# Performance work log

Hardware: AMD Instinct MI355X
Metric: run time of the kernel (lower is better)

Reference implementation:

```python
import jax, jax.numpy as jnp
import numpy as np

NUM_HEADS = 4
EPS = 1e-5  # GroupNorm default eps


def setup_inputs() -> dict:
    key = jax.random.key(0)
    ks = jax.random.split(key, 4)
    B, T, C, H, W = 4, 8, 128, 96, 96
    x = jax.random.normal(ks[0], (B, T, C, H, W), jnp.float32)
    pos_enc = jax.random.normal(ks[1], (1, 16, C, 1, 1), jnp.float32) * 0.02
    norm_w = jnp.ones((C,), jnp.float32)
    norm_b = jnp.zeros((C,), jnp.float32)
    qkv_w = jax.random.normal(ks[2], (3 * C, C), jnp.float32) * (1.0 / np.sqrt(C))
    proj_w = jax.random.normal(ks[3], (C, C), jnp.float32) * (1.0 / np.sqrt(C))
    return {"x": x, "pos_enc": pos_enc, "norm_w": norm_w, "norm_b": norm_b,
            "qkv_w": qkv_w, "proj_w": proj_w}


def reference(x, pos_enc, norm_w, norm_b, qkv_w, proj_w):
    B, T, C, H, W = x.shape
    nh = NUM_HEADS
    hd = C // nh
    scale = hd ** -0.5

    x = x + pos_enc[:, :T]

    # GroupNorm(1, C): normalize over (C,H,W) per (B,T) sample, biased var
    mean = x.mean(axis=(2, 3, 4), keepdims=True)
    var = x.var(axis=(2, 3, 4), keepdims=True)
    xn = (x - mean) * jax.lax.rsqrt(var + EPS)
    xn = xn * norm_w[None, None, :, None, None] + norm_b[None, None, :, None, None]

    # 1x1 conv -> matmul over channel dim; d = 3C
    qkv = jnp.einsum('btchw,dc->btdhw', xn, qkv_w)
    qkv = qkv.reshape(B, T, 3, nh, hd, H, W)
    q, k, v = qkv[:, :, 0], qkv[:, :, 1], qkv[:, :, 2]  # [B,T,nh,hd,H,W]

    # per-pixel temporal attention: scores [B,nh,H,W,T,T]
    attn = jnp.einsum('btndhw,bsndhw->bnhwts', q, k) * scale
    attn = jax.nn.softmax(attn, axis=-1)

    # only the last query row is kept (out[..., -1, :] in the original)
    out = jnp.einsum('bnhws,bsndhw->bndhw', attn[..., -1, :], v)
    out = out.reshape(B, C, H, W)
    return jnp.einsum('bchw,dc->bdhw', out, proj_w)
```

## Files before the change

kernel.cpp:

```cpp
#include <hip/hip_runtime.h>
#include <math.h>

#define BB 4
#define TT 8
#define CC 128
#define HWW 9216
#define NPG 1179648.0f
#define EPS 1e-5f
#define SCALE 0.17677669529663687f
#define SCALE2 0.2550181765195206f

#define WS_PART 0
#define WS_A    8192
#define WS_B    12288

typedef __attribute__((ext_vector_type(4))) float f32x4;

__global__ __launch_bounds__(256) void stats_kernel(
    const float* __restrict__ x, const float* __restrict__ pe,
    float* __restrict__ part)
{
    const int bid = blockIdx.x;
    const int g = bid >> 7, c = bid & 127;
    const int t = g & 7;
    const int tid = threadIdx.x;
    const float pec = pe[t * CC + c];
    const float4* row = (const float4*)(x + ((size_t)g * CC + c) * HWW);
    float s1 = 0.f, s2 = 0.f;
    #pragma unroll
    for (int i = 0; i < 9; ++i) {
        float4 v = row[tid + i * 256];
        float a = v.x + pec, b = v.y + pec, cc2 = v.z + pec, d = v.w + pec;
        s1 += (a + b) + (cc2 + d);
        s2 += (a * a + b * b) + (cc2 * cc2 + d * d);
    }
    for (int off = 32; off; off >>= 1) {
        s1 += __shfl_down(s1, off);
        s2 += __shfl_down(s2, off);
    }
    __shared__ float red[8];
    const int wid = tid >> 6, lane = tid & 63;
    if (lane == 0) { red[wid] = s1; red[4 + wid] = s2; }
    __syncthreads();
    if (tid == 0) {
        part[bid * 2 + 0] = red[0] + red[1] + red[2] + red[3];
        part[bid * 2 + 1] = red[4] + red[5] + red[6] + red[7];
    }
}

__global__ __launch_bounds__(128) void finalize_kernel(
    const float* __restrict__ pe, const float* __restrict__ nw,
    const float* __restrict__ nb, float* ws)
{
    const int g = blockIdx.x;
    const int c = threadIdx.x;
    const float* part = ws + WS_PART + g * 256;
    float s1 = part[c * 2 + 0];
    float s2 = part[c * 2 + 1];
    for (int off = 32; off; off >>= 1) {
        s1 += __shfl_down(s1, off);
        s2 += __shfl_down(s2, off);
    }
    __shared__ float r[4];
    const int wid = c >> 6, lane = c & 63;
    if (lane == 0) { r[wid] = s1; r[2 + wid] = s2; }
    __syncthreads();
    const float inv = 1.0f / NPG;
    const float mean = (r[0] + r[1]) * inv;
    const float var  = (r[2] + r[3]) * inv - mean * mean;
    const float rstd = rsqrtf(var + EPS);
    const int t = g & 7;
    const float a = rstd * nw[c];
    ws[WS_A + g * CC + c] = a;
    ws[WS_B + g * CC + c] = (pe[t * CC + c] - mean) * a + nb[c];
}

__global__ __launch_bounds__(1024, 4) void fused7_kernel(
    const float* __restrict__ x, const float* __restrict__ ws,
    const float* __restrict__ qkv_w, const float* __restrict__ proj_w,
    float* __restrict__ out)
{
    __shared__ __align__(16) float bufA[CC * 64];
    __shared__ __align__(16) float bufB[CC * 64];

    const int tid  = threadIdx.x;
    const int lane = tid & 63;
    const int w    = tid >> 6;
    const int wu   = __builtin_amdgcn_readfirstlane(w);
    const int n    = wu >> 2;
    const int hq   = wu & 3;
    const int b    = blockIdx.y;
    const int hw0  = blockIdx.x * 64;

    const int r  = tid >> 3;
    const int k8 = (tid & 7) * 8;

    float ar[8], br[8];
    #pragma unroll
    for (int t = 0; t < 8; ++t) {
        ar[t] = ws[WS_A + (b * TT + t) * CC + r];
        br[t] = ws[WS_B + (b * TT + t) * CC + r];
    }

    const float* xrow = x + ((size_t)(b * TT) * CC + r) * HWW + hw0 + k8;

    f32x4 rg0, rg1;
    auto ldtile = [&](int t) {
        const float* p = xrow + (size_t)t * CC * HWW;
        rg0 = *(const f32x4*)(p);
        rg1 = *(const f32x4*)(p + 4);
    };
    auto wrtile = [&](float a, float bb2, float* dst) {
        f32x4 f0, f1;
        f0.x = fmaf(rg0.x, a, bb2); f0.y = fmaf(rg0.y, a, bb2);
        f0.z = fmaf(rg0.z, a, bb2); f0.w = fmaf(rg0.w, a, bb2);
        f1.x = fmaf(rg1.x, a, bb2); f1.y = fmaf(rg1.y, a, bb2);
        f1.z = fmaf(rg1.z, a, bb2); f1.w = fmaf(rg1.w, a, bb2);
        *(f32x4*)&dst[r * 64 + k8]     = f0;
        *(f32x4*)&dst[r * 64 + k8 + 4] = f1;
    };

    float u[32];
    auto score = [&](const float* buf) {
        float s0 = 0.f, s1 = 0.f, s2 = 0.f, s3 = 0.f;
        #pragma unroll
        for (int j = 0; j < 32; j += 4) {
            s0 = fmaf(u[j + 0], buf[(hq * 32 + j + 0) * 64 + lane], s0);
            s1 = fmaf(u[j + 1], buf[(hq * 32 + j + 1) * 64 + lane], s1);
            s2 = fmaf(u[j + 2], buf[(hq * 32 + j + 2) * 64 + lane], s2);
            s3 = fmaf(u[j + 3], buf[(hq * 32 + j + 3) * 64 + lane], s3);
        }
        return (s0 + s1) + (s2 + s3);
    };

    ldtile(7);
    wrtile(ar[7], br[7], bufA);
    __syncthreads();

    {
        const float* Wq = qkv_w + (n * 32 + hq * 8) * CC;
        float q7[8] = {0.f,0.f,0.f,0.f,0.f,0.f,0.f,0.f};
        for (int c0 = 0; c0 < CC; c0 += 8) {
            float xv[8];
            #pragma unroll
            for (int i = 0; i < 8; ++i)
                xv[i] = bufA[(c0 + i) * 64 + lane];
            #pragma unroll
            for (int d = 0; d < 8; ++d) {
                #pragma unroll
                for (int i = 0; i < 8; ++i)
                    q7[d] = fmaf(Wq[d * CC + c0 + i], xv[i], q7[d]);
            }
        }
        #pragma unroll
        for (int d = 0; d < 8; ++d)
            bufB[(n * 32 + hq * 8 + d) * 64 + lane] = q7[d];
    }
    __syncthreads();

    ldtile(0);

    #pragma unroll
    for (int j = 0; j < 32; ++j) u[j] = 0.f;
    {
        const float* Wk = qkv_w + (CC + n * 32) * CC + hq * 32;
        for (int d = 0; d < 32; ++d) {
            const float qv = bufB[(n * 32 + d) * 64 + lane];
            #pragma unroll
            for (int j = 0; j < 32; ++j)
                u[j] = fmaf(Wk[d * CC + j], qv, u[j]);
        }
    }
    __syncthreads();

    float ps[8];
    wrtile(ar[0], br[0], bufB);
    ps[7] = score(bufA);
    ldtile(1);
    __syncthreads();

    #pragma unroll
    for (int t = 0; t < 7; ++t) {
        const float* curb = (t & 1) ? bufA : bufB;
        float* othb = (t & 1) ? bufB : bufA;
        if (t < 6) {
            if (t == 0) wrtile(ar[1], br[1], othb);
            if (t == 1) wrtile(ar[2], br[2], othb);
            if (t == 2) wrtile(ar[3], br[3], othb);
            if (t == 3) wrtile(ar[4], br[4], othb);
            if (t == 4) wrtile(ar[5], br[5], othb);
            if (t == 5) wrtile(ar[6], br[6], othb);
        }
        if (t < 5) ldtile(t + 2);
        ps[t] = score(curb);
        __syncthreads();
    }

    ldtile(0);
    #pragma unroll
    for (int t = 0; t < 8; ++t)
        bufA[(wu * 8 + t) * 64 + lane] = ps[t];
    __syncthreads();

    float wt[8];
    {
        float sreg[8];
        #pragma unroll
        for (int t = 0; t < 8; ++t)
            sreg[t] = (bufA[((n * 4 + 0) * 8 + t) * 64 + lane] +
                       bufA[((n * 4 + 1) * 8 + t) * 64 + lane]) +
                      (bufA[((n * 4 + 2) * 8 + t) * 64 + lane] +
                       bufA[((n * 4 + 3) * 8 + t) * 64 + lane]);
        float m = fmaxf(fmaxf(fmaxf(sreg[0], sreg[1]), fmaxf(sreg[2], sreg[3])),
                        fmaxf(fmaxf(sreg[4], sreg[5]), fmaxf(sreg[6], sreg[7])));
        float l = 0.f;
        #pragma unroll
        for (int t = 0; t < 8; ++t) { wt[t] = exp2f((sreg[t] - m) * SCALE2); l += wt[t]; }
        const float invl = 1.0f / l;
        #pragma unroll
        for (int t = 0; t < 8; ++t) wt[t] *= invl;
    }
    __syncthreads();

    float xb[32];
    #pragma unroll
    for (int j = 0; j < 32; ++j) xb[j] = 0.f;
    #pragma unroll
    for (int t = 0; t < 8; ++t) {
        float* wb = (t & 1) ? bufB : bufA;
        {
            if (t == 0) wrtile(ar[0], br[0], wb);
            if (t == 1) wrtile(ar[1], br[1], wb);
            if (t == 2) wrtile(ar[2], br[2], wb);
            if (t == 3) wrtile(ar[3], br[3], wb);
            if (t == 4) wrtile(ar[4], br[4], wb);
            if (t == 5) wrtile(ar[5], br[5], wb);
            if (t == 6) wrtile(ar[6], br[6], wb);
            if (t == 7) wrtile(ar[7], br[7], wb);
        }
        if (t < 7) ldtile(t + 1);
        if (t >= 1) {
            const float* rb = (t & 1) ? bufA : bufB;
            const float wc = wt[t - 1];
            #pragma unroll
            for (int j = 0; j < 32; ++j)
                xb[j] = fmaf(rb[(hq * 32 + j) * 64 + lane], wc, xb[j]);
        }
        __syncthreads();
    }
    {
        const float wc = wt[7];
        #pragma unroll
        for (int j = 0; j < 32; ++j)
            xb[j] = fmaf(bufB[(hq * 32 + j) * 64 + lane], wc, xb[j]);
    }
    __syncthreads();

    {
        const float* Wv = qkv_w + (2 * CC + n * 32) * CC + hq * 32;
        float vprev[8];
        #pragma unroll
        for (int gi = 0; gi < 4; ++gi) {
            float vp[8];
            #pragma unroll
            for (int d = 0; d < 8; ++d) {
                float s0 = 0.f, s1 = 0.f, s2 = 0.f, s3 = 0.f;
                const float* Wr = Wv + (gi * 8 + d) * CC;
                #pragma unroll
                for (int c = 0; c < 32; c += 4) {
                    s0 = fmaf(Wr[c + 0], xb[c + 0], s0);
                    s1 = fmaf(Wr[c + 1], xb[c + 1], s1);
                    s2 = fmaf(Wr[c + 2], xb[c + 2], s2);
                    s3 = fmaf(Wr[c + 3], xb[c + 3], s3);
                }
                vp[d] = (s0 + s1) + (s2 + s3);
            }
            if (hq == 1) {
                #pragma unroll
                for (int d = 0; d < 8; ++d)
                    bufB[(n * 32 + gi * 8 + d) * 64 + lane] = vp[d];
            }
            if (hq == 3) {
                #pragma unroll
                for (int d = 0; d < 8; ++d)
                    bufA[(n * 32 + gi * 8 + d) * 64 + lane] = vp[d];
            }
            if (gi > 0) {
                if (hq == 0) {
                    #pragma unroll
                    for (int d = 0; d < 8; ++d)
                        bufB[(n * 32 + (gi - 1) * 8 + d) * 64 + lane] += vprev[d];
                }
                if (hq == 2) {
                    #pragma unroll
                    for (int d = 0; d < 8; ++d)
                        bufA[(n * 32 + (gi - 1) * 8 + d) * 64 + lane] += vprev[d];
                }
            }
            #pragma unroll
            for (int d = 0; d < 8; ++d) vprev[d] = vp[d];
            __syncthreads();
        }
        if (hq == 0) {
            #pragma unroll
            for (int d = 0; d < 8; ++d)
                bufB[(n * 32 + 24 + d) * 64 + lane] += vprev[d];
        }
        if (hq == 2) {
            #pragma unroll
            for (int d = 0; d < 8; ++d)
                bufA[(n * 32 + 24 + d) * 64 + lane] += vprev[d];
        }
    }
    __syncthreads();

    float y[8];
    #pragma unroll
    for (int e = 0; e < 8; ++e) y[e] = 0.f;
    for (int c0 = 0; c0 < CC; c0 += 16) {
        float vv[16];
        #pragma unroll
        for (int i = 0; i < 16; ++i)
            vv[i] = bufB[(c0 + i) * 64 + lane] + bufA[(c0 + i) * 64 + lane];
        #pragma unroll
        for (int e = 0; e < 8; ++e) {
            const float* Pr = proj_w + (wu * 8 + e) * CC + c0;
            #pragma unroll
            for (int i = 0; i < 16; ++i)
                y[e] = fmaf(Pr[i], vv[i], y[e]);
        }
    }
    const size_t ob = (size_t)(b * CC + wu * 8) * HWW + hw0 + lane;
    #pragma unroll
    for (int e = 0; e < 8; ++e)
        out[ob + (size_t)e * HWW] = y[e];
}

extern "C" void kernel_launch(void* const* d_in, const int* in_sizes, int n_in,
                              void* d_out, int out_size, void* d_ws, size_t ws_size,
                              hipStream_t stream) {
    const float* x      = (const float*)d_in[0];
    const float* pe     = (const float*)d_in[1];
    const float* nw     = (const float*)d_in[2];
    const float* nb     = (const float*)d_in[3];
    const float* qkv_w  = (const float*)d_in[4];
    const float* proj_w = (const float*)d_in[5];
    float* out = (float*)d_out;
    float* ws  = (float*)d_ws;

    stats_kernel<<<4096, 256, 0, stream>>>(x, pe, ws + WS_PART);
    finalize_kernel<<<32, 128, 0, stream>>>(pe, nw, nb, ws);
    fused7_kernel<<<dim3(HWW / 64, BB), 1024, 0, stream>>>(x, ws, qkv_w, proj_w, out);
}
```

Before: 413.9 us.

## Transpose LDS tiles to pixel-major with XOR swizzle and vectorized reads

Shared-memory tiles change from channel-major to pixel-major rows of 128 channels, with an XOR swizzle on 4-float groups. Every consumer (score, q/k projections, weighted sum, v partial sums, output projection) now reads 128-bit vectors instead of scalar LDS loads. The per-timestep normalization coefficients are loaded alongside each x tile instead of kept in 16 registers. The launch-bounds occupancy hint goes from 4 to 8, which presses register allocation. The tile writes become eight scattered scalar stores, which may add bank conflicts on the write side.

```diff
diff --git a/kernel.cpp b/kernel.cpp
--- a/kernel.cpp
+++ b/kernel.cpp
@@ -75,13 +75,13 @@
     ws[WS_B + g * CC + c] = (pe[t * CC + c] - mean) * a + nb[c];
 }
 
-__global__ __launch_bounds__(1024, 4) void fused7_kernel(
+__global__ __launch_bounds__(1024, 8) void fused8_kernel(
     const float* __restrict__ x, const float* __restrict__ ws,
     const float* __restrict__ qkv_w, const float* __restrict__ proj_w,
     float* __restrict__ out)
 {
-    __shared__ __align__(16) float bufA[CC * 64];
-    __shared__ __align__(16) float bufB[CC * 64];
+    __shared__ __align__(16) float bufA[64 * CC];
+    __shared__ __align__(16) float bufB[64 * CC];
 
     const int tid  = threadIdx.x;
     const int lane = tid & 63;
@@ -92,69 +92,76 @@
     const int b    = blockIdx.y;
     const int hw0  = blockIdx.x * 64;
 
+    const int pg   = (lane >> 3) & 7;
+    const int rowb = lane * 128;
+
     const int r  = tid >> 3;
     const int k8 = (tid & 7) * 8;
 
-    float ar[8], br[8];
-    #pragma unroll
-    for (int t = 0; t < 8; ++t) {
-        ar[t] = ws[WS_A + (b * TT + t) * CC + r];
-        br[t] = ws[WS_B + (b * TT + t) * CC + r];
-    }
-
     const float* xrow = x + ((size_t)(b * TT) * CC + r) * HWW + hw0 + k8;
+    const float* Arow = ws + WS_A + (b * TT) * CC + r;
+    const float* Brow = ws + WS_B + (b * TT) * CC + r;
 
     f32x4 rg0, rg1;
+    float sa, sb;
     auto ldtile = [&](int t) {
         const float* p = xrow + (size_t)t * CC * HWW;
         rg0 = *(const f32x4*)(p);
         rg1 = *(const f32x4*)(p + 4);
+        sa = Arow[t * CC];
+        sb = Brow[t * CC];
     };
-    auto wrtile = [&](float a, float bb2, float* dst) {
-        f32x4 f0, f1;
-        f0.x = fmaf(rg0.x, a, bb2); f0.y = fmaf(rg0.y, a, bb2);
-        f0.z = fmaf(rg0.z, a, bb2); f0.w = fmaf(rg0.w, a, bb2);
-        f1.x = fmaf(rg1.x, a, bb2); f1.y = fmaf(rg1.y, a, bb2);
-        f1.z = fmaf(rg1.z, a, bb2); f1.w = fmaf(rg1.w, a, bb2);
-        *(f32x4*)&dst[r * 64 + k8]     = f0;
-        *(f32x4*)&dst[r * 64 + k8 + 4] = f1;
+    auto wrtile = [&](float* dst) {
+        const int base = k8 * 128 + ((((r >> 2) ^ ((k8 >> 3) & 7)) << 2) | (r & 3));
+        dst[base + 0 * 128] = fmaf(rg0.x, sa, sb);
+        dst[base + 1 * 128] = fmaf(rg0.y, sa, sb);
+        dst[base + 2 * 128] = fmaf(rg0.z, sa, sb);
+        dst[base + 3 * 128] = fmaf(rg0.w, sa, sb);
+        dst[base + 4 * 128] = fmaf(rg1.x, sa, sb);
+        dst[base + 5 * 128] = fmaf(rg1.y, sa, sb);
+        dst[base + 6 * 128] = fmaf(rg1.z, sa, sb);
+        dst[base + 7 * 128] = fmaf(rg1.w, sa, sb);
     };
 
     float u[32];
     auto score = [&](const float* buf) {
         float s0 = 0.f, s1 = 0.f, s2 = 0.f, s3 = 0.f;
         #pragma unroll
-        for (int j = 0; j < 32; j += 4) {
-            s0 = fmaf(u[j + 0], buf[(hq * 32 + j + 0) * 64 + lane], s0);
-            s1 = fmaf(u[j + 1], buf[(hq * 32 + j + 1) * 64 + lane], s1);
-            s2 = fmaf(u[j + 2], buf[(hq * 32 + j + 2) * 64 + lane], s2);
-            s3 = fmaf(u[j + 3], buf[(hq * 32 + j + 3) * 64 + lane], s3);
+        for (int jj = 0; jj < 8; ++jj) {
+            f32x4 v = *(const f32x4*)&buf[rowb + (((hq * 8 + jj) ^ pg) << 2)];
+            s0 = fmaf(u[jj * 4 + 0], v.x, s0);
+            s1 = fmaf(u[jj * 4 + 1], v.y, s1);
+            s2 = fmaf(u[jj * 4 + 2], v.z, s2);
+            s3 = fmaf(u[jj * 4 + 3], v.w, s3);
         }
         return (s0 + s1) + (s2 + s3);
     };
 
     ldtile(7);
-    wrtile(ar[7], br[7], bufA);
+    wrtile(bufA);
     __syncthreads();
 
     {
         const float* Wq = qkv_w + (n * 32 + hq * 8) * CC;
         float q7[8] = {0.f,0.f,0.f,0.f,0.f,0.f,0.f,0.f};
-        for (int c0 = 0; c0 < CC; c0 += 8) {
-            float xv[8];
-            #pragma unroll
-            for (int i = 0; i < 8; ++i)
-                xv[i] = bufA[(c0 + i) * 64 + lane];
+        #pragma unroll
+        for (int cc = 0; cc < 32; ++cc) {
+            f32x4 xv = *(const f32x4*)&bufA[rowb + ((cc ^ pg) << 2)];
             #pragma unroll
             for (int d = 0; d < 8; ++d) {
-                #pragma unroll
-                for (int i = 0; i < 8; ++i)
-                    q7[d] = fmaf(Wq[d * CC + c0 + i], xv[i], q7[d]);
-            }
-        }
-        #pragma unroll
-        for (int d = 0; d < 8; ++d)
-            bufB[(n * 32 + hq * 8 + d) * 64 + lane] = q7[d];
+                const float* Wr = Wq + d * CC + cc * 4;
+                q7[d] = fmaf(Wr[0], xv.x, q7[d]);
+                q7[d] = fmaf(Wr[1], xv.y, q7[d]);
+                q7[d] = fmaf(Wr[2], xv.z, q7[d]);
+                q7[d] = fmaf(Wr[3], xv.w, q7[d]);
+            }
+        }
+        const int c0 = n * 8 + hq * 2;
+        f32x4 e0, e1;
+        e0.x = q7[0]; e0.y = q7[1]; e0.z = q7[2]; e0.w = q7[3];
+        e1.x = q7[4]; e1.y = q7[5]; e1.z = q7[6]; e1.w = q7[7];
+        *(f32x4*)&bufB[rowb + ((c0 ^ pg) << 2)]       = e0;
+        *(f32x4*)&bufB[rowb + (((c0 + 1) ^ pg) << 2)] = e1;
     }
     __syncthreads();
 
@@ -164,17 +171,26 @@
     for (int j = 0; j < 32; ++j) u[j] = 0.f;
     {
         const float* Wk = qkv_w + (CC + n * 32) * CC + hq * 32;
-        for (int d = 0; d < 32; ++d) {
-            const float qv = bufB[(n * 32 + d) * 64 + lane];
-            #pragma unroll
-            for (int j = 0; j < 32; ++j)
-                u[j] = fmaf(Wk[d * CC + j], qv, u[j]);
+        #pragma unroll
+        for (int qq = 0; qq < 8; ++qq) {
+            f32x4 qv = *(const f32x4*)&bufB[rowb + (((n * 8 + qq) ^ pg) << 2)];
+            const float* W0 = Wk + (qq * 4 + 0) * CC;
+            const float* W1 = Wk + (qq * 4 + 1) * CC;
+            const float* W2 = Wk + (qq * 4 + 2) * CC;
+            const float* W3 = Wk + (qq * 4 + 3) * CC;
+            #pragma unroll
+            for (int j = 0; j < 32; ++j) {
+                u[j] = fmaf(W0[j], qv.x, u[j]);
+                u[j] = fmaf(W1[j], qv.y, u[j]);
+                u[j] = fmaf(W2[j], qv.z, u[j]);
+                u[j] = fmaf(W3[j], qv.w, u[j]);
+            }
         }
     }
     __syncthreads();
 
     float ps[8];
-    wrtile(ar[0], br[0], bufB);
+    wrtile(bufB);
     ps[7] = score(bufA);
     ldtile(1);
     __syncthreads();
@@ -183,34 +199,36 @@
     for (int t = 0; t < 7; ++t) {
         const float* curb = (t & 1) ? bufA : bufB;
         float* othb = (t & 1) ? bufB : bufA;
-        if (t < 6) {
-            if (t == 0) wrtile(ar[1], br[1], othb);
-            if (t == 1) wrtile(ar[2], br[2], othb);
-            if (t == 2) wrtile(ar[3], br[3], othb);
-            if (t == 3) wrtile(ar[4], br[4], othb);
-            if (t == 4) wrtile(ar[5], br[5], othb);
-            if (t == 5) wrtile(ar[6], br[6], othb);
-        }
+        if (t < 6) wrtile(othb);
         if (t < 5) ldtile(t + 2);
         ps[t] = score(curb);
         __syncthreads();
     }
 
     ldtile(0);
-    #pragma unroll
-    for (int t = 0; t < 8; ++t)
-        bufA[(wu * 8 + t) * 64 + lane] = ps[t];
+    {
+        const int p0 = wu * 2;
+        f32x4 e0, e1;
+        e0.x = ps[0]; e0.y = ps[1]; e0.z = ps[2]; e0.w = ps[3];
+        e1.x = ps[4]; e1.y = ps[5]; e1.z = ps[6]; e1.w = ps[7];
+        *(f32x4*)&bufA[rowb + ((p0 ^ pg) << 2)]       = e0;
+        *(f32x4*)&bufA[rowb + (((p0 + 1) ^ pg) << 2)] = e1;
+    }
     __syncthreads();
 
     float wt[8];
     {
+        float wq[32];
+        #pragma unroll
+        for (int qq = 0; qq < 8; ++qq) {
+            f32x4 v = *(const f32x4*)&bufA[rowb + (((n * 8 + qq) ^ pg) << 2)];
+            wq[qq * 4 + 0] = v.x; wq[qq * 4 + 1] = v.y;
+            wq[qq * 4 + 2] = v.z; wq[qq * 4 + 3] = v.w;
+        }
         float sreg[8];
         #pragma unroll
         for (int t = 0; t < 8; ++t)
-            sreg[t] = (bufA[((n * 4 + 0) * 8 + t) * 64 + lane] +
-                       bufA[((n * 4 + 1) * 8 + t) * 64 + lane]) +
-                      (bufA[((n * 4 + 2) * 8 + t) * 64 + lane] +
-                       bufA[((n * 4 + 3) * 8 + t) * 64 + lane]);
+            sreg[t] = (wq[t] + wq[8 + t]) + (wq[16 + t] + wq[24 + t]);
         float m = fmaxf(fmaxf(fmaxf(sreg[0], sreg[1]), fmaxf(sreg[2], sreg[3])),
                         fmaxf(fmaxf(sreg[4], sreg[5]), fmaxf(sreg[6], sreg[7])));
         float l = 0.f;
@@ -228,31 +246,32 @@
     #pragma unroll
     for (int t = 0; t < 8; ++t) {
         float* wb = (t & 1) ? bufB : bufA;
-        {
-            if (t == 0) wrtile(ar[0], br[0], wb);
-            if (t == 1) wrtile(ar[1], br[1], wb);
-            if (t == 2) wrtile(ar[2], br[2], wb);
-            if (t == 3) wrtile(ar[3], br[3], wb);
-            if (t == 4) wrtile(ar[4], br[4], wb);
-            if (t == 5) wrtile(ar[5], br[5], wb);
-            if (t == 6) wrtile(ar[6], br[6], wb);
-            if (t == 7) wrtile(ar[7], br[7], wb);
-        }
+        wrtile(wb);
         if (t < 7) ldtile(t + 1);
         if (t >= 1) {
             const float* rb = (t & 1) ? bufA : bufB;
             const float wc = wt[t - 1];
             #pragma unroll
-            for (int j = 0; j < 32; ++j)
-                xb[j] = fmaf(rb[(hq * 32 + j) * 64 + lane], wc, xb[j]);
+            for (int jj = 0; jj < 8; ++jj) {
+                f32x4 v = *(const f32x4*)&rb[rowb + (((hq * 8 + jj) ^ pg) << 2)];
+                xb[jj * 4 + 0] = fmaf(v.x, wc, xb[jj * 4 + 0]);
+                xb[jj * 4 + 1] = fmaf(v.y, wc, xb[jj * 4 + 1]);
+                xb[jj * 4 + 2] = fmaf(v.z, wc, xb[jj * 4 + 2]);
+                xb[jj * 4 + 3] = fmaf(v.w, wc, xb[jj * 4 + 3]);
+            }
         }
         __syncthreads();
     }
     {
         const float wc = wt[7];
         #pragma unroll
-        for (int j = 0; j < 32; ++j)
-            xb[j] = fmaf(bufB[(hq * 32 + j) * 64 + lane], wc, xb[j]);
+        for (int jj = 0; jj < 8; ++jj) {
+            f32x4 v = *(const f32x4*)&bufB[rowb + (((hq * 8 + jj) ^ pg) << 2)];
+            xb[jj * 4 + 0] = fmaf(v.x, wc, xb[jj * 4 + 0]);
+            xb[jj * 4 + 1] = fmaf(v.y, wc, xb[jj * 4 + 1]);
+            xb[jj * 4 + 2] = fmaf(v.z, wc, xb[jj * 4 + 2]);
+            xb[jj * 4 + 3] = fmaf(v.w, wc, xb[jj * 4 + 3]);
+        }
     }
     __syncthreads();
 
@@ -275,41 +294,38 @@
                 }
                 vp[d] = (s0 + s1) + (s2 + s3);
             }
-            if (hq == 1) {
-                #pragma unroll
-                for (int d = 0; d < 8; ++d)
-                    bufB[(n * 32 + gi * 8 + d) * 64 + lane] = vp[d];
-            }
-            if (hq == 3) {
-                #pragma unroll
-                for (int d = 0; d < 8; ++d)
-                    bufA[(n * 32 + gi * 8 + d) * 64 + lane] = vp[d];
-            }
-            if (gi > 0) {
-                if (hq == 0) {
-                    #pragma unroll
-                    for (int d = 0; d < 8; ++d)
-                        bufB[(n * 32 + (gi - 1) * 8 + d) * 64 + lane] += vprev[d];
-                }
-                if (hq == 2) {
-                    #pragma unroll
-                    for (int d = 0; d < 8; ++d)
-                        bufA[(n * 32 + (gi - 1) * 8 + d) * 64 + lane] += vprev[d];
-                }
+            const int q0 = n * 8 + gi * 2;
+            if (hq == 1 || hq == 3) {
+                float* dst = (hq == 1) ? bufB : bufA;
+                f32x4 w0, w1;
+                w0.x = vp[0]; w0.y = vp[1]; w0.z = vp[2]; w0.w = vp[3];
+                w1.x = vp[4]; w1.y = vp[5]; w1.z = vp[6]; w1.w = vp[7];
+                *(f32x4*)&dst[rowb + ((q0 ^ pg) << 2)]       = w0;
+                *(f32x4*)&dst[rowb + (((q0 + 1) ^ pg) << 2)] = w1;
+            }
+            if (gi > 0 && (hq == 0 || hq == 2)) {
+                float* dst = (hq == 0) ? bufB : bufA;
+                const int m0 = n * 8 + (gi - 1) * 2;
+                f32x4 c0 = *(const f32x4*)&dst[rowb + ((m0 ^ pg) << 2)];
+                f32x4 c1 = *(const f32x4*)&dst[rowb + (((m0 + 1) ^ pg) << 2)];
+                c0.x += vprev[0]; c0.y += vprev[1]; c0.z += vprev[2]; c0.w += vprev[3];
+                c1.x += vprev[4]; c1.y += vprev[5]; c1.z += vprev[6]; c1.w += vprev[7];
+                *(f32x4*)&dst[rowb + ((m0 ^ pg) << 2)]       = c0;
+                *(f32x4*)&dst[rowb + (((m0 + 1) ^ pg) << 2)] = c1;
             }
             #pragma unroll
             for (int d = 0; d < 8; ++d) vprev[d] = vp[d];
             __syncthreads();
         }
-        if (hq == 0) {
-            #pragma unroll
-            for (int d = 0; d < 8; ++d)
-                bufB[(n * 32 + 24 + d) * 64 + lane] += vprev[d];
-        }
-        if (hq == 2) {
-            #pragma unroll
-            for (int d = 0; d < 8; ++d)
-                bufA[(n * 32 + 24 + d) * 64 + lane] += vprev[d];
+        if (hq == 0 || hq == 2) {
+            float* dst = (hq == 0) ? bufB : bufA;
+            const int m0 = n * 8 + 6;
+            f32x4 c0 = *(const f32x4*)&dst[rowb + ((m0 ^ pg) << 2)];
+            f32x4 c1 = *(const f32x4*)&dst[rowb + (((m0 + 1) ^ pg) << 2)];
+            c0.x += vprev[0]; c0.y += vprev[1]; c0.z += vprev[2]; c0.w += vprev[3];
+            c1.x += vprev[4]; c1.y += vprev[5]; c1.z += vprev[6]; c1.w += vprev[7];
+            *(f32x4*)&dst[rowb + ((m0 ^ pg) << 2)]       = c0;
+            *(f32x4*)&dst[rowb + (((m0 + 1) ^ pg) << 2)] = c1;
         }
     }
     __syncthreads();
@@ -317,17 +333,19 @@
     float y[8];
     #pragma unroll
     for (int e = 0; e < 8; ++e) y[e] = 0.f;
-    for (int c0 = 0; c0 < CC; c0 += 16) {
-        float vv[16];
-        #pragma unroll
-        for (int i = 0; i < 16; ++i)
-            vv[i] = bufB[(c0 + i) * 64 + lane] + bufA[(c0 + i) * 64 + lane];
+    #pragma unroll
+    for (int cc = 0; cc < 32; ++cc) {
+        f32x4 va = *(const f32x4*)&bufB[rowb + ((cc ^ pg) << 2)];
+        f32x4 vb = *(const f32x4*)&bufA[rowb + ((cc ^ pg) << 2)];
+        const float v0 = va.x + vb.x, v1 = va.y + vb.y;
+        const float v2 = va.z + vb.z, v3 = va.w + vb.w;
         #pragma unroll
         for (int e = 0; e < 8; ++e) {
-            const float* Pr = proj_w + (wu * 8 + e) * CC + c0;
-            #pragma unroll
-            for (int i = 0; i < 16; ++i)
-                y[e] = fmaf(Pr[i], vv[i], y[e]);
+            const float* Pr = proj_w + (wu * 8 + e) * CC + cc * 4;
+            y[e] = fmaf(Pr[0], v0, y[e]);
+            y[e] = fmaf(Pr[1], v1, y[e]);
+            y[e] = fmaf(Pr[2], v2, y[e]);
+            y[e] = fmaf(Pr[3], v3, y[e]);
         }
     }
     const size_t ob = (size_t)(b * CC + wu * 8) * HWW + hw0 + lane;
@@ -350,5 +368,5 @@
 
     stats_kernel<<<4096, 256, 0, stream>>>(x, pe, ws + WS_PART);
     finalize_kernel<<<32, 128, 0, stream>>>(pe, nw, nb, ws);
-    fused7_kernel<<<dim3(HWW / 64, BB), 1024, 0, stream>>>(x, ws, qkv_w, proj_w, out);
+    fused8_kernel<<<dim3(HWW / 64, BB), 1024, 0, stream>>>(x, ws, qkv_w, proj_w, out);
 }
```

After: 1.610 ms. +288.9%, slower.
